# Performance work log

Measured on AMD Instinct MI355X. Metric: run time of the kernel, lower is better.

## Reference

```python
import jax, jax.numpy as jnp
import numpy as np
from jax import lax

B = 2; C = 256; NH = 8; NP = 4; NUM_LAYERS = 6; FFN = 1024
IN_SIZES = (512, 1024, 2048)
LVL_SHAPES = ((64, 64), (32, 32), (16, 16), (8, 8), (4, 4))
NL = len(LVL_SHAPES); DH = C // NH
N = sum(h * w for h, w in LVL_SHAPES)  # 5456 tokens over the pyramid


def _ln(x, g, b):
    m = x.mean(-1, keepdims=True)
    v = x.var(-1, keepdims=True)
    return (x - m) * lax.rsqrt(v + 1e-5) * g + b


def _gn(x, g, b, groups=8):
    Bb, Cc, Hh, Ww = x.shape
    xr = x.reshape(Bb, groups, Cc // groups, Hh, Ww)
    m = xr.mean((2, 3, 4), keepdims=True)
    v = xr.var((2, 3, 4), keepdims=True)
    xr = (xr - m) * lax.rsqrt(v + 1e-5)
    return xr.reshape(Bb, Cc, Hh, Ww) * g[None, :, None, None] + b[None, :, None, None]


def _conv(x, w, b, stride, pad):
    y = lax.conv_general_dilated(x, w, (stride, stride), [(pad, pad), (pad, pad)],
                                 dimension_numbers=('NCHW', 'OIHW', 'NCHW'))
    return y + b[None, :, None, None]


def _priors():
    # normalized (cx, cy) anchor centers per pyramid location
    pr = []
    for (fh, fw) in LVL_SHAPES:
        cy = (jnp.arange(fh, dtype=jnp.float32) + 0.5) / fh
        cx = (jnp.arange(fw, dtype=jnp.float32) + 0.5) / fw
        gy, gx = jnp.meshgrid(cy, cx, indexing='ij')
        pr.append(jnp.stack([gx, gy], -1).reshape(-1, 2))
    return jnp.concatenate(pr, 0)  # [N,2]


def _sample(vl, loc, fh, fw):
    # vl: [B,NH,S_l,DH] flattened level values; loc: [B,N,NH,NP,2] in [0,1]
    x = loc[..., 0] * fw - 0.5
    y = loc[..., 1] * fh - 0.5
    x0 = jnp.floor(x); y0 = jnp.floor(y)
    lx = x - x0; ly = y - y0

    def gather(xi, yi):
        inb = ((xi >= 0) & (xi <= fw - 1) & (yi >= 0) & (yi <= fh - 1)).astype(vl.dtype)
        xc = jnp.clip(xi, 0, fw - 1).astype(jnp.int32)
        yc = jnp.clip(yi, 0, fh - 1).astype(jnp.int32)
        idx = (yc * fw + xc).transpose(0, 2, 1, 3).reshape(B, NH, N * NP)
        g = jnp.take_along_axis(vl, idx[..., None], axis=2)  # [B,NH,N*NP,DH]
        g = g.reshape(B, NH, N, NP, DH).transpose(0, 2, 1, 3, 4)  # [B,N,NH,NP,DH]
        return g * inb[..., None]

    return (gather(x0, y0) * ((1 - lx) * (1 - ly))[..., None]
            + gather(x0 + 1, y0) * (lx * (1 - ly))[..., None]
            + gather(x0, y0 + 1) * ((1 - lx) * ly)[..., None]
            + gather(x0 + 1, y0 + 1) * (lx * ly)[..., None])


def _attn_layer(x, priors, g1, b1_, woff, boff, watt, batt, wval, bval, wout, bout):
    q = _ln(x, g1, b1_)
    off = (q @ woff + boff).reshape(B, N, NH, NL, NP, 2)
    att = jax.nn.softmax((q @ watt + batt).reshape(B, N, NH, NL * NP), axis=-1)
    att = att.reshape(B, N, NH, NL, NP)
    val = (q @ wval + bval).reshape(B, N, NH, DH)
    normz = jnp.array([[w, h] for (h, w) in LVL_SHAPES], jnp.float32)  # (W,H) per level
    loc = priors[None, :, None, None, None, :] + off / normz[None, None, None, :, None, :]
    out = jnp.zeros((B, N, NH, DH), x.dtype)
    start = 0
    for l, (fh, fw) in enumerate(LVL_SHAPES):
        vl = val[:, start:start + fh * fw].transpose(0, 2, 1, 3)  # [B,NH,S_l,DH]
        s = _sample(vl, loc[:, :, :, l], fh, fw)  # [B,N,NH,NP,DH]
        out = out + (s * att[:, :, :, l, :, None]).sum(3)
        start += fh * fw
    return x + out.reshape(B, N, C) @ wout + bout


def _ffn(x, g2, b2_, w1, b1_, w2, b2_2):
    h = jax.nn.relu(_ln(x, g2, b2_) @ w1 + b1_)
    return x + h @ w2 + b2_2


def _forward(in_map0, in_map1, in_map2, pw0, pb0, pw1, pb1, pw2, pb2,
             buw0, bub0, gng, gnb, buw1, bub1,
             ln1g, ln1b, woff, boff, watt, batt, wval, bval, wout, bout,
             ln2g, ln2b, w1, b1, w2, b2):
    maps = [_conv(in_map0, pw0, pb0, 1, 0), _conv(in_map1, pw1, pb1, 1, 0), _conv(in_map2, pw2, pb2, 1, 0)]
    m = _conv(in_map2, buw0, bub0, 2, 1)  # bottom-up from raw C5 (2048ch)
    maps.append(m)
    m = _conv(jax.nn.relu(_gn(m, gng, gnb)), buw1, bub1, 2, 1)
    maps.append(m)
    feats = jnp.concatenate([mm.reshape(B, C, -1).transpose(0, 2, 1) for mm in maps], axis=1)  # [B,N,C]
    priors = _priors()
    for i in range(NUM_LAYERS):
        feats = _attn_layer(feats, priors, ln1g[i], ln1b[i], woff[i], boff[i],
                            watt[i], batt[i], wval[i], bval[i], wout[i], bout[i])
        feats = _ffn(feats, ln2g[i], ln2b[i], w1[i], b1[i], w2[i], b2[i])
    return feats


def setup_inputs():
    key = jax.random.key(0)
    ks = list(jax.random.split(key, 40)); ki = iter(ks)
    def rn(shape, s=0.02):
        return jax.random.normal(next(ki), shape, jnp.float32) * s
    inp = {}
    for i, (cs, (h, w)) in enumerate(zip(IN_SIZES, LVL_SHAPES[:3])):
        inp[f"in_map{i}"] = jax.random.normal(next(ki), (B, cs, h, w), jnp.float32)
    for i, cs in enumerate(IN_SIZES):
        inp[f"pw{i}"] = rn((C, cs, 1, 1)); inp[f"pb{i}"] = jnp.zeros((C,), jnp.float32)
    inp["buw0"] = rn((C, IN_SIZES[-1], 3, 3)); inp["bub0"] = jnp.zeros((C,), jnp.float32)
    inp["gng"] = jnp.ones((C,), jnp.float32); inp["gnb"] = jnp.zeros((C,), jnp.float32)
    inp["buw1"] = rn((C, C, 3, 3)); inp["bub1"] = jnp.zeros((C,), jnp.float32)
    LYR = NUM_LAYERS
    inp["ln1g"] = jnp.ones((LYR, C), jnp.float32); inp["ln1b"] = jnp.zeros((LYR, C), jnp.float32)
    inp["woff"] = rn((LYR, C, NH * NL * NP * 2), 0.01)
    th = np.arange(NH) * (2.0 * np.pi / NH)
    grid = np.stack([np.cos(th), np.sin(th)], -1)
    grid = grid / np.abs(grid).max(-1, keepdims=True)  # [NH,2]
    boff = np.tile(grid[:, None, None, :], (1, NL, NP, 1)) * (np.arange(NP) + 1)[None, None, :, None]
    inp["boff"] = jnp.tile(jnp.asarray(boff.reshape(-1), jnp.float32)[None], (LYR, 1))
    inp["watt"] = rn((LYR, C, NH * NL * NP), 0.01); inp["batt"] = jnp.zeros((LYR, NH * NL * NP), jnp.float32)
    inp["wval"] = rn((LYR, C, C)); inp["bval"] = jnp.zeros((LYR, C), jnp.float32)
    inp["wout"] = rn((LYR, C, C)); inp["bout"] = jnp.zeros((LYR, C), jnp.float32)
    inp["ln2g"] = jnp.ones((LYR, C), jnp.float32); inp["ln2b"] = jnp.zeros((LYR, C), jnp.float32)
    inp["w1"] = rn((LYR, C, FFN)); inp["b1"] = jnp.zeros((LYR, FFN), jnp.float32)
    inp["w2"] = rn((LYR, FFN, C)); inp["b2"] = jnp.zeros((LYR, C), jnp.float32)
    return inp


def reference(in_map0, in_map1, in_map2, pw0, pb0, pw1, pb1, pw2, pb2,
              buw0, bub0, gng, gnb, buw1, bub1,
              ln1g, ln1b, woff, boff, watt, batt, wval, bval, wout, bout,
              ln2g, ln2b, w1, b1, w2, b2):
    feats = _forward(in_map0, in_map1, in_map2, pw0, pb0, pw1, pb1, pw2, pb2,
                     buw0, bub0, gng, gnb, buw1, bub1,
                     ln1g, ln1b, woff, boff, watt, batt, wval, bval, wout, bout,
                     ln2g, ln2b, w1, b1, w2, b2)
    outs = []
    start = 0
    for (fh, fw) in LVL_SHAPES:
        outs.append(feats[:, start:start + fh * fw].transpose(0, 2, 1).reshape(B, C, fh, fw))
        start += fh * fw
    return tuple(outs)
```

## Files before the change

### kernel.cpp

```cpp
#include <hip/hip_runtime.h>
#include <cstdint>

typedef long long i64;
typedef unsigned short u16;
typedef __attribute__((ext_vector_type(8))) short short8;
typedef __attribute__((ext_vector_type(8))) unsigned short us8;
typedef __attribute__((ext_vector_type(4))) float f32x4;

#define NTOK 5456
#define BNROWS 10912
#define NLAYERS 6

__device__ __forceinline__ u16 f2bf(float f) {
  unsigned u = __float_as_uint(f);
  return (u16)((u + 0x7FFFu + ((u >> 16) & 1u)) >> 16);
}
__device__ __forceinline__ float bf2f(u16 h) {
  return __uint_as_float(((unsigned)h) << 16);
}

template<int BNT>
__global__ __launch_bounds__(256) void mgemm_k(
    const u16* __restrict__ A, const u16* __restrict__ B, int K,
    float* __restrict__ C, float* __restrict__ C2, u16* __restrict__ C16, i64 sCm,
    const float* __restrict__ bias, int relu, int addres, int qkv,
    int M, int N, int mbsh, i64 bCz,
    int KS, float* __restrict__ part)
{
  constexpr int NW = BNT / 32;
  __shared__ u16 Asm[2][128 * 64];
  __shared__ u16 Bsm[2][BNT * 64];
  int tid = threadIdx.x;

  int bx = blockIdx.x, by = blockIdx.y;
  int gx = gridDim.x, gy = gridDim.y;
  int nwg = gx * gy;
  if (KS == 1 && nwg >= 16) {
    int lin = bx + gx * by;
    int xcd = lin & 7, k = lin >> 3;
    int q = nwg >> 3, r = nwg & 7;
    int f = (xcd < r) ? (xcd * (q + 1) + k) : (r * (q + 1) + (xcd - r) * q + k);
    bx = f / gy;
    by = f - bx * gy;
  }
  int m0 = bx * 128, n0 = by * BNT;

  int ks = blockIdx.z;
  int Kc = K / KS;
  int k0 = ks * Kc;
  int lane = tid & 63, w = tid >> 6;
  int wr = w >> 1, wc = w & 1;
  int r16 = lane & 15, g = lane >> 4;

  f32x4 acc[4][NW];
#pragma unroll
  for (int mi = 0; mi < 4; mi++)
#pragma unroll
    for (int nj = 0; nj < NW; nj++) acc[mi][nj] = (f32x4){0.f, 0.f, 0.f, 0.f};

  const u16* Ag = A + (i64)m0 * K + k0;
  const u16* Bg = B + (i64)n0 * K + k0;
  int nt = Kc >> 6;

  auto stage = [&](int buf, int kt) {
#pragma unroll
    for (int r = 0; r < 4; r++) {
      int s = r * 256 + tid;
      int row = s >> 3, c = s & 7;
      int cs = ((c ^ (row & 7)) << 3);
      __builtin_amdgcn_global_load_lds(
          (const __attribute__((address_space(1))) void*)(Ag + (i64)row * K + kt + cs),
          (__attribute__((address_space(3))) void*)(&Asm[buf][(r * 256 + (w << 6)) << 3]),
          16, 0, 0);
    }
#pragma unroll
    for (int r = 0; r < NW; r++) {
      int s = r * 256 + tid;
      int row = s >> 3, c = s & 7;
      int cs = ((c ^ (row & 7)) << 3);
      __builtin_amdgcn_global_load_lds(
          (const __attribute__((address_space(1))) void*)(Bg + (i64)row * K + kt + cs),
          (__attribute__((address_space(3))) void*)(&Bsm[buf][(r * 256 + (w << 6)) << 3]),
          16, 0, 0);
    }
  };

  stage(0, 0);
  __syncthreads();
  for (int t = 0; t < nt; t++) {
    int cur = t & 1;
    if (t + 1 < nt) stage(cur ^ 1, (t + 1) << 6);
#pragma unroll
    for (int h = 0; h < 2; h++) {
      short8 av[4], bv[NW];
#pragma unroll
      for (int mi = 0; mi < 4; mi++) {
        int row = wr * 64 + mi * 16 + r16;
        av[mi] = *(const short8*)&Asm[cur][row * 64 + ((((h << 2) + g) ^ (row & 7)) << 3)];
      }
#pragma unroll
      for (int nj = 0; nj < NW; nj++) {
        int row = wc * (NW * 16) + nj * 16 + r16;
        bv[nj] = *(const short8*)&Bsm[cur][row * 64 + ((((h << 2) + g) ^ (row & 7)) << 3)];
      }
#pragma unroll
      for (int mi = 0; mi < 4; mi++)
#pragma unroll
        for (int nj = 0; nj < NW; nj++)
          acc[mi][nj] = __builtin_amdgcn_mfma_f32_16x16x32_bf16(
              av[mi], bv[nj], acc[mi][nj], 0, 0, 0);
    }
    __syncthreads();
  }

  if (KS > 1) {
#pragma unroll
    for (int mi = 0; mi < 4; mi++)
#pragma unroll
      for (int nj = 0; nj < NW; nj++)
#pragma unroll
        for (int r = 0; r < 4; r++) {
          int grow = m0 + wr * 64 + mi * 16 + g * 4 + r;
          int gcol = n0 + wc * (NW * 16) + nj * 16 + r16;
          if (grow < M) part[((i64)ks * M + grow) * N + gcol] = acc[mi][nj][r];
        }
  } else if (qkv) {
    u16* off16 = (u16*)C;
    u16* att16 = (u16*)C2;
#pragma unroll
    for (int mi = 0; mi < 4; mi++)
#pragma unroll
      for (int nj = 0; nj < NW; nj++)
#pragma unroll
        for (int r = 0; r < 4; r++) {
          int grow = m0 + wr * 64 + mi * 16 + g * 4 + r;
          int gcol = n0 + wc * (NW * 16) + nj * 16 + r16;
          if (grow < M) {
            float v = acc[mi][nj][r] + bias[gcol];
            if (gcol < 320) off16[(i64)grow * 320 + gcol] = f2bf(v);
            else if (gcol < 480) att16[(i64)grow * 160 + (gcol - 320)] = f2bf(v);
            else if (gcol < 736) C16[(i64)grow * 256 + (gcol - 480)] = f2bf(v);
          }
        }
  } else {
    float bv[NW];
    int gc0 = n0 + wc * (NW * 16) + r16;
#pragma unroll
    for (int nj = 0; nj < NW; nj++)
      bv[nj] = bias ? bias[gc0 + nj * 16] : 0.f;
    int mask = (1 << mbsh) - 1;
#pragma unroll
    for (int mi = 0; mi < 4; mi++) {
#pragma unroll
      for (int r = 0; r < 4; r++) {
        int grow = m0 + wr * 64 + mi * 16 + g * 4 + r;
        if (grow >= M) continue;
        i64 rowb = (i64)(grow >> mbsh) * bCz + (i64)(grow & mask) * sCm;
#pragma unroll
        for (int nj = 0; nj < NW; nj++) {
          int gcol = gc0 + nj * 16;
          if (gcol >= N) continue;
          float v = acc[mi][nj][r] + bv[nj];
          if (relu) v = fmaxf(v, 0.f);
          i64 ci = rowb + gcol;
          if (C16) C16[ci] = f2bf(v);
          else {
            if (addres) v += C[ci];
            C[ci] = v;
          }
        }
      }
    }
  }
}

__global__ __launch_bounds__(512, 1) void ffn_fused_k(
    float* __restrict__ feats, const u16* __restrict__ w1n,
    const u16* __restrict__ w2n, const float* __restrict__ b1,
    const float* __restrict__ b2, const float* __restrict__ lng,
    const float* __restrict__ lnb, int M)
{
  __shared__ u16 B1s[2][64 * 256];
  __shared__ u16 B2s[2][256 * 64];
  __shared__ u16 Hs[64 * 88];
  __shared__ float b1s[1024];
  u16* As = &B1s[1][0];

  int tid = threadIdx.x;
  int lane = tid & 63, w = tid >> 6;
  int wr = w >> 1, wc = w & 1;
  int r16 = lane & 15, g = lane >> 4;
  int m0 = blockIdx.x * 64;

  auto stageW = [&](int buf, int ch) {
#pragma unroll
    for (int r = 0; r < 4; r++) {
      int s = r * 512 + tid;
      int row = s >> 5, c = s & 31;
      int cs = ((c ^ (row & 7)) << 3);
      __builtin_amdgcn_global_load_lds(
          (const __attribute__((address_space(1))) void*)(w1n + (i64)(ch * 64 + row) * 256 + cs),
          (__attribute__((address_space(3))) void*)(&B1s[buf][(r * 512 + (w << 6)) << 3]),
          16, 0, 0);
    }
#pragma unroll
    for (int r = 0; r < 4; r++) {
      int s = r * 512 + tid;
      int row = s >> 3, c = s & 7;
      int cs = ((c ^ (row & 7)) << 3);
      __builtin_amdgcn_global_load_lds(
          (const __attribute__((address_space(1))) void*)(w2n + (i64)row * 1024 + ch * 64 + cs),
          (__attribute__((address_space(3))) void*)(&B2s[buf][(r * 512 + (w << 6)) << 3]),
          16, 0, 0);
    }
  };

  stageW(0, 0);
  for (int i = tid; i < 1024; i += 512) b1s[i] = b1[i];

  {
    int rw = tid >> 3, c0 = (tid & 7) * 32;
    const float* fr = feats + (i64)(m0 + rw) * 256 + c0;
    float4 x[8];
    float s = 0.f, ss = 0.f;
#pragma unroll
    for (int j = 0; j < 8; j++) {
      x[j] = ((const float4*)fr)[j];
      s += x[j].x + x[j].y + x[j].z + x[j].w;
      ss += x[j].x * x[j].x + x[j].y * x[j].y + x[j].z * x[j].z + x[j].w * x[j].w;
    }
#pragma unroll
    for (int o = 1; o <= 4; o <<= 1) { s += __shfl_xor(s, o); ss += __shfl_xor(ss, o); }
    float mean = s * (1.f / 256.f);
    float rs = rsqrtf(ss * (1.f / 256.f) - mean * mean + 1e-5f);
    const float4* gp = (const float4*)(lng + c0);
    const float4* bp = (const float4*)(lnb + c0);
#pragma unroll
    for (int j = 0; j < 8; j += 2) {
      float4 g0 = gp[j], g1 = gp[j + 1];
      float4 b0 = bp[j], b1_ = bp[j + 1];
      us8 o;
      o[0] = f2bf((x[j].x - mean) * rs * g0.x + b0.x);
      o[1] = f2bf((x[j].y - mean) * rs * g0.y + b0.y);
      o[2] = f2bf((x[j].z - mean) * rs * g0.z + b0.z);
      o[3] = f2bf((x[j].w - mean) * rs * g0.w + b0.w);
      o[4] = f2bf((x[j + 1].x - mean) * rs * g1.x + b1_.x);
      o[5] = f2bf((x[j + 1].y - mean) * rs * g1.y + b1_.y);
      o[6] = f2bf((x[j + 1].z - mean) * rs * g1.z + b1_.z);
      o[7] = f2bf((x[j + 1].w - mean) * rs * g1.w + b1_.w);
      int gr = (tid & 7) * 4 + (j >> 1);
      *(us8*)&As[rw * 256 + ((gr ^ (rw & 7)) << 3)] = o;
    }
  }
  __syncthreads();

  short8 av_all[8];
  {
    int row = wr * 16 + r16;
#pragma unroll
    for (int ks = 0; ks < 8; ks++)
      av_all[ks] = *(const short8*)&As[row * 256 + (((ks * 4 + g) ^ (row & 7)) << 3)];
  }
  __syncthreads();

  f32x4 acc2[8];
#pragma unroll
  for (int nj = 0; nj < 8; nj++) acc2[nj] = (f32x4){0.f, 0.f, 0.f, 0.f};

  int cur = 0;
  for (int ch = 0; ch < 16; ch++) {
    if (ch + 1 < 16) stageW(cur ^ 1, ch + 1);

    f32x4 acc1[2];
#pragma unroll
    for (int nj = 0; nj < 2; nj++) acc1[nj] = (f32x4){0.f, 0.f, 0.f, 0.f};
#pragma unroll
    for (int ks = 0; ks < 8; ks++) {
      short8 bv[2];
#pragma unroll
      for (int nj = 0; nj < 2; nj++) {
        int row = wc * 32 + nj * 16 + r16;
        bv[nj] = *(const short8*)&B1s[cur][row * 256 + (((ks * 4 + g) ^ (row & 7)) << 3)];
      }
#pragma unroll
      for (int nj = 0; nj < 2; nj++)
        acc1[nj] = __builtin_amdgcn_mfma_f32_16x16x32_bf16(
            av_all[ks], bv[nj], acc1[nj], 0, 0, 0);
    }
#pragma unroll
    for (int nj = 0; nj < 2; nj++)
#pragma unroll
      for (int r = 0; r < 4; r++) {
        int hr = wr * 16 + g * 4 + r;
        int hc = wc * 32 + nj * 16 + r16;
        float v = acc1[nj][r] + b1s[ch * 64 + hc];
        Hs[hr * 88 + hc] = f2bf(fmaxf(v, 0.f));
      }
    __syncthreads();

#pragma unroll
    for (int hh = 0; hh < 2; hh++) {
      short8 av2 = *(const short8*)&Hs[(wr * 16 + r16) * 88 + hh * 32 + g * 8];
      short8 bv2[8];
#pragma unroll
      for (int nj = 0; nj < 8; nj++) {
        int n = wc * 128 + nj * 16 + r16;
        bv2[nj] = *(const short8*)&B2s[cur][n * 64 + (((hh * 4 + g) ^ (n & 7)) << 3)];
      }
#pragma unroll
      for (int nj = 0; nj < 8; nj++)
        acc2[nj] = __builtin_amdgcn_mfma_f32_16x16x32_bf16(
            av2, bv2[nj], acc2[nj], 0, 0, 0);
    }
    __syncthreads();
    cur ^= 1;
  }

#pragma unroll
  for (int r = 0; r < 4; r++) {
    int grow = m0 + wr * 16 + g * 4 + r;
    if (grow >= M) continue;
#pragma unroll
    for (int nj = 0; nj < 8; nj++) {
      int col = wc * 128 + nj * 16 + r16;
      i64 ci = (i64)grow * 256 + col;
      feats[ci] += acc2[nj][r] + b2[col];
    }
  }
}

__global__ void reduce_k(const float* __restrict__ part, float* __restrict__ C,
    const float* __restrict__ bias, int mbsh, i64 bCz, i64 sCm, int M, int N, int KS)
{
  int idx = blockIdx.x * 256 + threadIdx.x;
  if (idx >= M * N) return;
  int m = idx / N, n = idx - m * N;
  float v = bias ? bias[n] : 0.f;
  for (int ks = 0; ks < KS; ks++) v += part[((i64)ks * M + m) * N + n];
  C[(i64)(m >> mbsh) * bCz + (i64)(m & ((1 << mbsh) - 1)) * sCm + n] = v;
}

__global__ void cvt_w_pro_k(const float* __restrict__ pw0, const float* __restrict__ pw1,
    const float* __restrict__ pw2, const float* __restrict__ buw0,
    const float* __restrict__ buw1, u16* __restrict__ dst)
{
  int idx = blockIdx.x * 256 + threadIdx.x;
  if (idx >= 6225920) return;
  float v;
  if (idx < 131072) v = pw0[idx];
  else if (idx < 393216) v = pw1[idx - 131072];
  else if (idx < 917504) v = pw2[idx - 393216];
  else if (idx < 5636096) v = buw0[idx - 917504];
  else v = buw1[idx - 5636096];
  dst[idx] = f2bf(v);
}

__global__ void cvt_w_layer_k(const float* __restrict__ woff, const float* __restrict__ watt,
    const float* __restrict__ wval, const float* __restrict__ wout,
    const float* __restrict__ w1, const float* __restrict__ w2, u16* __restrict__ dst)
{
  int L = blockIdx.y;
  int o = blockIdx.x * 256 + threadIdx.x;
  if (o >= 786432) return;
  u16* d = dst + (i64)L * 786432;
  float v;
  if (o < 196608) {
    int n = o >> 8, k = o & 255;
    if (n < 320) v = woff[(i64)L * 81920 + k * 320 + n];
    else if (n < 480) v = watt[(i64)L * 40960 + k * 160 + (n - 320)];
    else if (n < 736) v = wval[(i64)L * 65536 + k * 256 + (n - 480)];
    else v = 0.f;
  } else if (o < 262144) {
    int o2 = o - 196608; int n = o2 >> 8, k = o2 & 255;
    v = wout[(i64)L * 65536 + k * 256 + n];
  } else if (o < 524288) {
    int o2 = o - 262144; int n = o2 >> 8, k = o2 & 255;
    v = w1[(i64)L * 262144 + (i64)k * 1024 + n];
  } else {
    int o2 = o - 524288; int n = o2 >> 10, k = o2 & 1023;
    v = w2[(i64)L * 262144 + (i64)k * 256 + n];
  }
  d[o] = f2bf(v);
}

__global__ void cvt_bias_k(const float* __restrict__ boff, const float* __restrict__ batt,
    const float* __restrict__ bval, float* __restrict__ bq)
{
  int idx = blockIdx.x * 256 + threadIdx.x;
  if (idx >= NLAYERS * 768) return;
  int L = idx / 768, n = idx - L * 768;
  float v;
  if (n < 320) v = boff[(i64)L * 320 + n];
  else if (n < 480) v = batt[(i64)L * 160 + (n - 320)];
  else if (n < 736) v = bval[(i64)L * 256 + (n - 480)];
  else v = 0.f;
  bq[idx] = v;
}

__global__ void cvt_a_proj_k(const float* __restrict__ in, u16* __restrict__ out,
                             int P, int K)
{
  i64 o = (i64)blockIdx.x * 256 + threadIdx.x;
  if (o >= (i64)2 * P * K) return;
  int m = (int)(o / K), k = (int)(o % K);
  int b = m / P, p = m - b * P;
  out[o] = f2bf(in[((i64)b * K + k) * P + p]);
}

__global__ void im2col_bf16_k(const float* __restrict__ in, u16* __restrict__ out,
    int Cin, int Hin, int Win, int Ho, int Wo)
{
  int Kk = Cin * 9;
  i64 total = (i64)2 * Ho * Wo * Kk;
  i64 o = (i64)blockIdx.x * 256 + threadIdx.x;
  if (o >= total) return;
  int k = (int)(o % Kk);
  int m = (int)(o / Kk);
  int hw = Ho * Wo;
  int b = m / hw, pix = m - b * hw;
  int oy = pix / Wo, ox = pix - oy * Wo;
  int ci = k / 9, r = k - ci * 9;
  int ky = r / 3, kx = r - ky * 3;
  int iy = oy * 2 - 1 + ky, ix = ox * 2 - 1 + kx;
  float v = 0.f;
  if (iy >= 0 && iy < Hin && ix >= 0 && ix < Win)
    v = in[(((i64)b * Cin + ci) * Hin + iy) * Win + ix];
  out[o] = f2bf(v);
}

__global__ void gn_relu_k(const float* __restrict__ feats, float* __restrict__ y,
    const float* __restrict__ g, const float* __restrict__ bt)
{
  int grp = blockIdx.x, b = blockIdx.y;
  int tid = threadIdx.x;
  const float* fb = feats + ((i64)b * NTOK + 5376) * 256 + grp * 32;
  float s = 0.f, ss = 0.f;
  for (int i = tid; i < 2048; i += 256) {
    int cl = i >> 6, p = i & 63;
    float v = fb[(i64)p * 256 + cl];
    s += v; ss += v * v;
  }
  __shared__ float sb[4], ssb[4];
#pragma unroll
  for (int o = 32; o > 0; o >>= 1) { s += __shfl_down(s, o); ss += __shfl_down(ss, o); }
  int wv = tid >> 6;
  if ((tid & 63) == 0) { sb[wv] = s; ssb[wv] = ss; }
  __syncthreads();
  float ts = sb[0] + sb[1] + sb[2] + sb[3];
  float tss = ssb[0] + ssb[1] + ssb[2] + ssb[3];
  float mean = ts * (1.f / 2048.f);
  float rs = rsqrtf(tss * (1.f / 2048.f) - mean * mean + 1e-5f);
  for (int i = tid; i < 2048; i += 256) {
    int cl = i >> 6, p = i & 63;
    int c = grp * 32 + cl;
    float v = (fb[(i64)p * 256 + cl] - mean) * rs * g[c] + bt[c];
    y[((i64)b * 256 + c) * 64 + p] = fmaxf(v, 0.f);
  }
}

__global__ __launch_bounds__(256) void ln_k(const float* __restrict__ x,
    u16* __restrict__ y, const float* __restrict__ g, const float* __restrict__ bt,
    int rows)
{
  int row = blockIdx.x * 4 + (threadIdx.x >> 6);
  if (row >= rows) return;
  int lane = threadIdx.x & 63;
  float4 v = ((const float4*)(x + (i64)row * 256))[lane];
  float s = v.x + v.y + v.z + v.w;
  float ss = v.x * v.x + v.y * v.y + v.z * v.z + v.w * v.w;
#pragma unroll
  for (int o = 32; o > 0; o >>= 1) { s += __shfl_down(s, o); ss += __shfl_down(ss, o); }
  s = __shfl(s, 0);
  ss = __shfl(ss, 0);
  float mean = s * (1.f / 256.f);
  float rs = rsqrtf(ss * (1.f / 256.f) - mean * mean + 1e-5f);
  float4 gg = ((const float4*)g)[lane];
  float4 bb = ((const float4*)bt)[lane];
  ushort4 o4;
  o4.x = f2bf((v.x - mean) * rs * gg.x + bb.x);
  o4.y = f2bf((v.y - mean) * rs * gg.y + bb.y);
  o4.z = f2bf((v.z - mean) * rs * gg.z + bb.z);
  o4.w = f2bf((v.w - mean) * rs * gg.w + bb.w);
  ((ushort4*)(y + (i64)row * 256))[lane] = o4;
}

__global__ __launch_bounds__(256) void dsample_k(
    const u16* __restrict__ val, const u16* __restrict__ off,
    const u16* __restrict__ att, u16* __restrict__ out)
{
  const int FH[5] = {64, 32, 16, 8, 4};
  const int ST[5] = {0, 4096, 5120, 5376, 5440};
  int bid = blockIdx.x;
  int chunk = (bid & 7) * 86 + (bid >> 3);
  if (chunk >= 682) return;
  int lane = threadIdx.x & 63;
  int half = lane >> 5;
  int l32 = lane & 31;
  int t = chunk * 8 + ((threadIdx.x >> 6) << 1) + half;
  int b = blockIdx.y;
  int h = l32 >> 2, d4 = l32 & 3;

  int lv;
  if (t < 4096)      lv = 0;
  else if (t < 5120) lv = 1;
  else if (t < 5376) lv = 2;
  else if (t < 5440) lv = 3;
  else               lv = 4;
  int loc = t - ST[lv];
  int sh = 6 - lv;
  int py = loc >> sh, px = loc - (py << sh);
  float inv = 1.f / (float)FH[lv];
  float prx = (px + 0.5f) * inv, pry = (py + 0.5f) * inv;
  i64 bt = (i64)b * NTOK + t;
  const u16* offp = off + bt * 320 + h * 40;
  const u16* attp = att + bt * 160 + h * 20;
  const u16* vbase = val + ((i64)b * NTOK) * 256 + h * 32 + d4 * 8;

  float own_a[5], own_fx[5], own_fy[5];
  int own_pk[5];
  float mx = -1e30f;
#pragma unroll
  for (int j = 0; j < 5; j++) {
    float lg = bf2f(attp[d4 + 4 * j]);
    own_a[j] = lg;
    mx = fmaxf(mx, lg);
  }
  mx = fmaxf(mx, __shfl_xor(mx, 1));
  mx = fmaxf(mx, __shfl_xor(mx, 2));
  float sum = 0.f;
#pragma unroll
  for (int j = 0; j < 5; j++) {
    float e = __expf(own_a[j] - mx);
    own_a[j] = e;
    sum += e;
  }
  sum += __shfl_xor(sum, 1);
  sum += __shfl_xor(sum, 2);
  float rinv = 1.f / sum;
#pragma unroll
  for (int j = 0; j < 5; j++) {
    int p = d4 + 4 * j;
    own_a[j] *= rinv;
    unsigned opk = *(const unsigned*)(offp + 2 * p);
    float ox = bf2f((u16)(opk & 0xFFFF));
    float oy = bf2f((u16)(opk >> 16));
    float sff = (float)(64 >> j);
    float xx = prx * sff + ox - 0.5f;
    float yy = pry * sff + oy - 0.5f;
    float xf = floorf(xx), yf = floorf(yy);
    own_fx[j] = xx - xf;
    own_fy[j] = yy - yf;
    own_pk[j] = (((int)yf) << 16) | (((int)xf) & 0xFFFF);
  }

  float acc[8] = {0.f, 0.f, 0.f, 0.f, 0.f, 0.f, 0.f, 0.f};
#pragma unroll
  for (int p = 0; p < 20; p++) {
    const int j = p >> 2;
    const int sf = FH[j], st = ST[j];
    int src = (half << 5) | (h << 2) | (p & 3);
    float wa = __shfl(own_a[j], src);
    float fx = __shfl(own_fx[j], src);
    float fy = __shfl(own_fy[j], src);
    int pk = __shfl(own_pk[j], src);
    int x0 = (pk << 16) >> 16;
    int y0 = pk >> 16;
    float gx0 = wa - wa * fx, gx1 = wa * fx;
    float w00 = gx0 - gx0 * fy, w01 = gx0 * fy;
    float w10 = gx1 - gx1 * fy, w11 = gx1 * fy;
    bool xin0 = (x0 >= 0) & (x0 < sf), xin1 = (x0 + 1 >= 0) & (x0 + 1 < sf);
    bool yin0 = (y0 >= 0) & (y0 < sf), yin1 = (y0 + 1 >= 0) & (y0 + 1 < sf);
    int ibase = st + y0 * sf + x0;
#define FMA8(W, IDX) { \
      us8 v = *(const us8*)(vbase + (i64)(IDX) * 256); \
      acc[0] = fmaf(W, bf2f(v[0]), acc[0]); acc[1] = fmaf(W, bf2f(v[1]), acc[1]); \
      acc[2] = fmaf(W, bf2f(v[2]), acc[2]); acc[3] = fmaf(W, bf2f(v[3]), acc[3]); \
      acc[4] = fmaf(W, bf2f(v[4]), acc[4]); acc[5] = fmaf(W, bf2f(v[5]), acc[5]); \
      acc[6] = fmaf(W, bf2f(v[6]), acc[6]); acc[7] = fmaf(W, bf2f(v[7]), acc[7]); }
    if (xin0 & yin0) FMA8(w00, ibase);
    if (xin1 & yin0) FMA8(w10, ibase + 1);
    if (xin0 & yin1) FMA8(w01, ibase + sf);
    if (xin1 & yin1) FMA8(w11, ibase + sf + 1);
#undef FMA8
  }
  us8 o;
#pragma unroll
  for (int i = 0; i < 8; i++) o[i] = f2bf(acc[i]);
  *(us8*)(out + ((bt * 8 + h) * 32 + d4 * 8)) = o;
}

__global__ __launch_bounds__(256) void untranspose_all_k(
    const float* __restrict__ feats, float* __restrict__ out)
{
  int u = blockIdx.x;
  int pt0, start, S; i64 ooff;
  if (u < 128)      { pt0 = u;       start = 0;    S = 4096; ooff = 0; }
  else if (u < 160) { pt0 = u - 128; start = 4096; S = 1024; ooff = 2097152; }
  else if (u < 168) { pt0 = u - 160; start = 5120; S = 256;  ooff = 2621440; }
  else if (u < 170) { pt0 = u - 168; start = 5376; S = 64;   ooff = 2752512; }
  else              { pt0 = 0;       start = 5440; S = 16;   ooff = 2785280; }
  __shared__ float tile[32][33];
  int pt = pt0 * 32, ct = blockIdx.y * 32, b = blockIdx.z;
  int tx = threadIdx.x & 31, ty = threadIdx.x >> 5;
  for (int i = ty; i < 32; i += 8) {
    int p = pt + i;
    tile[i][tx] = (p < S) ? feats[((i64)b * NTOK + start + p) * 256 + ct + tx] : 0.f;
  }
  __syncthreads();
  for (int i = ty; i < 32; i += 8) {
    int c = ct + i, p = pt + tx;
    if (p < S) out[ooff + ((i64)b * 256 + c) * S + p] = tile[tx][i];
  }
}

extern "C" void kernel_launch(void* const* d_in, const int* in_sizes, int n_in,
                              void* d_out, int out_size, void* d_ws, size_t ws_size,
                              hipStream_t stream)
{
  const float* in0  = (const float*)d_in[0];
  const float* in1  = (const float*)d_in[1];
  const float* in2  = (const float*)d_in[2];
  const float* pw0  = (const float*)d_in[3];
  const float* pb0  = (const float*)d_in[4];
  const float* pw1  = (const float*)d_in[5];
  const float* pb1  = (const float*)d_in[6];
  const float* pw2  = (const float*)d_in[7];
  const float* pb2  = (const float*)d_in[8];
  const float* buw0 = (const float*)d_in[9];
  const float* bub0 = (const float*)d_in[10];
  const float* gng  = (const float*)d_in[11];
  const float* gnb  = (const float*)d_in[12];
  const float* buw1 = (const float*)d_in[13];
  const float* bub1 = (const float*)d_in[14];
  const float* ln1g = (const float*)d_in[15];
  const float* ln1b = (const float*)d_in[16];
  const float* woff = (const float*)d_in[17];
  const float* boff = (const float*)d_in[18];
  const float* watt = (const float*)d_in[19];
  const float* batt = (const float*)d_in[20];
  const float* wval = (const float*)d_in[21];
  const float* bval = (const float*)d_in[22];
  const float* wout = (const float*)d_in[23];
  const float* bout = (const float*)d_in[24];
  const float* ln2g = (const float*)d_in[25];
  const float* ln2b = (const float*)d_in[26];
  const float* w1   = (const float*)d_in[27];
  const float* b1   = (const float*)d_in[28];
  const float* w2   = (const float*)d_in[29];
  const float* b2   = (const float*)d_in[30];
  float* out = (float*)d_out;

  const i64 TC = (i64)NTOK * 256;

  float* ws    = (float*)d_ws;
  float* feats = ws;
  u16*   qb    = (u16*)(feats + 2793472);
  u16*   valb  = qb + 2818048;
  u16*   sampb = valb + 2818048;
  float* U     = (float*)(sampb + 2818048);
  u16*   off16 = (u16*)U;
  u16*   att16 = off16 + 3491840;
  u16*   abuf  = (u16*)U;
  float* part  = U + 2097152;
  u16*   wb    = (u16*)(U + 5637120);
  float* bqkv  = (float*)(wb + 10944512);
  float* m4gn  = bqkv + 4608;

  auto mg128 = [&](dim3 grid, const u16* A, const u16* B, int K,
                   float* C, float* C2, u16* C16, i64 sCm, const float* bias,
                   int relu, int addres, int qkv, int M, int N, int mbsh, i64 bCz, int KS) {
    mgemm_k<128><<<grid, dim3(256), 0, stream>>>(A, B, K, C, C2, C16, sCm, bias,
        relu, addres, qkv, M, N, mbsh, bCz, KS, part);
  };
  auto mg64 = [&](dim3 grid, const u16* A, const u16* B, int K,
                  float* C, u16* C16, i64 sCm, const float* bias,
                  int relu, int addres, int M, int N, int mbsh, i64 bCz, int KS) {
    mgemm_k<64><<<grid, dim3(256), 0, stream>>>(A, B, K, C, nullptr, C16, sCm, bias,
        relu, addres, 0, M, N, mbsh, bCz, KS, part);
  };

  cvt_w_pro_k<<<dim3(24320), dim3(256), 0, stream>>>(pw0, pw1, pw2, buw0, buw1, wb);
  cvt_w_layer_k<<<dim3(3072, NLAYERS), dim3(256), 0, stream>>>(
      woff, watt, wval, wout, w1, w2, wb + 6225920);
  cvt_bias_k<<<dim3(18), dim3(256), 0, stream>>>(boff, batt, bval, bqkv);

  cvt_a_proj_k<<<dim3(16384), dim3(256), 0, stream>>>(in0, abuf, 4096, 512);
  mg64(dim3(64, 4, 1), abuf, wb, 512, feats, nullptr, 256, pb0, 0, 0,
       8192, 256, 12, TC, 1);
  cvt_a_proj_k<<<dim3(8192), dim3(256), 0, stream>>>(in1, abuf, 1024, 1024);
  mg64(dim3(16, 4, 2), abuf, wb + 131072, 1024, nullptr, nullptr, 256, nullptr, 0, 0,
       2048, 256, 10, 0, 2);
  reduce_k<<<dim3(2048), dim3(256), 0, stream>>>(part, feats + (i64)4096 * 256, pb1,
      10, TC, 256, 2048, 256, 2);
  cvt_a_proj_k<<<dim3(4096), dim3(256), 0, stream>>>(in2, abuf, 256, 2048);
  mg64(dim3(4, 4, 4), abuf, wb + 393216, 2048, nullptr, nullptr, 256, nullptr, 0, 0,
       512, 256, 8, 0, 4);
  reduce_k<<<dim3(512), dim3(256), 0, stream>>>(part, feats + (i64)5120 * 256, pb2,
      8, TC, 256, 512, 256, 4);

  im2col_bf16_k<<<dim3(9216), dim3(256), 0, stream>>>(in2, abuf, 2048, 16, 16, 8, 8);
  mg64(dim3(1, 4, 16), abuf, wb + 917504, 18432, nullptr, nullptr, 256, nullptr, 0, 0,
       128, 256, 6, 0, 16);
  reduce_k<<<dim3(128), dim3(256), 0, stream>>>(part, feats + (i64)5376 * 256, bub0,
      6, TC, 256, 128, 256, 16);

  gn_relu_k<<<dim3(8, 2), dim3(256), 0, stream>>>(feats, m4gn, gng, gnb);
  im2col_bf16_k<<<dim3(288), dim3(256), 0, stream>>>(m4gn, abuf, 256, 8, 8, 4, 4);
  mg64(dim3(1, 4, 4), abuf, wb + 5636096, 2304, nullptr, nullptr, 256, nullptr, 0, 0,
       32, 256, 4, 0, 4);
  reduce_k<<<dim3(32), dim3(256), 0, stream>>>(part, feats + (i64)5440 * 256, bub1,
      4, TC, 256, 32, 256, 4);

  for (int i = 0; i < NLAYERS; i++) {
    const u16* wbL = wb + 6225920 + (i64)i * 786432;
    ln_k<<<dim3(2728), dim3(256), 0, stream>>>(feats, qb,
        ln1g + (i64)i * 256, ln1b + (i64)i * 256, BNROWS);
    mg128(dim3(86, 6, 1), qb, wbL, 256, (float*)off16, (float*)att16, valb, 0,
          bqkv + (i64)i * 768, 0, 0, 1, BNROWS, 768, 14, 0, 1);
    dsample_k<<<dim3(688, 2), dim3(256), 0, stream>>>(valb, off16, att16, sampb);
    mg64(dim3(86, 4, 1), sampb, wbL + 196608, 256, feats, nullptr, 256,
         bout + (i64)i * 256, 0, 1, BNROWS, 256, 14, 0, 1);
    ffn_fused_k<<<dim3(171), dim3(512), 0, stream>>>(feats, wbL + 262144,
        wbL + 524288, b1 + (i64)i * 1024, b2 + (i64)i * 256,
        ln2g + (i64)i * 256, ln2b + (i64)i * 256, BNROWS);
  }

  untranspose_all_k<<<dim3(171, 8, 2), dim3(256), 0, stream>>>(feats, out);
  (void)in_sizes; (void)n_in; (void)out_size; (void)ws_size;
}
```

Baseline: 957.4 us.

## Compute full 64-wide hidden chunk per wave to drop mid-loop barrier in fused FFN

Each wave now computes all 64 hidden columns of its 16-row slice in the first FFN GEMM, using swapped MFMA operands so results come out transposed. The hidden tile is written to a private per-wave LDS region with packed 32-bit stores. This removes the block-wide __syncthreads between the two GEMMs. The cost is that the first GEMM's work is duplicated across the two wc waves, doubling its MFMAs and weight reads from LDS.

```diff
diff --git a/kernel.cpp b/kernel.cpp
--- a/kernel.cpp
+++ b/kernel.cpp
@@ -4,12 +4,14 @@
 typedef long long i64;
 typedef unsigned short u16;
 typedef __attribute__((ext_vector_type(8))) short short8;
+typedef __attribute__((ext_vector_type(4))) short short4v;
 typedef __attribute__((ext_vector_type(8))) unsigned short us8;
 typedef __attribute__((ext_vector_type(4))) float f32x4;
 
 #define NTOK 5456
 #define BNROWS 10912
 #define NLAYERS 6
+#define HSTR 68
 
 __device__ __forceinline__ u16 f2bf(float f) {
   unsigned u = __float_as_uint(f);
@@ -182,7 +184,7 @@
 {
   __shared__ u16 B1s[2][64 * 256];
   __shared__ u16 B2s[2][256 * 64];
-  __shared__ u16 Hs[64 * 88];
+  __shared__ u16 Hs[8 * 16 * HSTR];
   __shared__ float b1s[1024];
   u16* As = &B1s[1][0];
 
@@ -267,40 +269,49 @@
 #pragma unroll
   for (int nj = 0; nj < 8; nj++) acc2[nj] = (f32x4){0.f, 0.f, 0.f, 0.f};
 
+  u16* Hw = &Hs[w * 16 * HSTR];
   int cur = 0;
   for (int ch = 0; ch < 16; ch++) {
     if (ch + 1 < 16) stageW(cur ^ 1, ch + 1);
 
-    f32x4 acc1[2];
-#pragma unroll
-    for (int nj = 0; nj < 2; nj++) acc1[nj] = (f32x4){0.f, 0.f, 0.f, 0.f};
+    f32x4 acc1[4];
+#pragma unroll
+    for (int fb = 0; fb < 4; fb++) acc1[fb] = (f32x4){0.f, 0.f, 0.f, 0.f};
 #pragma unroll
     for (int ks = 0; ks < 8; ks++) {
-      short8 bv[2];
-#pragma unroll
-      for (int nj = 0; nj < 2; nj++) {
-        int row = wc * 32 + nj * 16 + r16;
-        bv[nj] = *(const short8*)&B1s[cur][row * 256 + (((ks * 4 + g) ^ (row & 7)) << 3)];
+      short8 wv[4];
+#pragma unroll
+      for (int fb = 0; fb < 4; fb++) {
+        int row = fb * 16 + r16;
+        wv[fb] = *(const short8*)&B1s[cur][row * 256 + (((ks * 4 + g) ^ (row & 7)) << 3)];
       }
 #pragma unroll
-      for (int nj = 0; nj < 2; nj++)
-        acc1[nj] = __builtin_amdgcn_mfma_f32_16x16x32_bf16(
-            av_all[ks], bv[nj], acc1[nj], 0, 0, 0);
-    }
-#pragma unroll
-    for (int nj = 0; nj < 2; nj++)
-#pragma unroll
-      for (int r = 0; r < 4; r++) {
-        int hr = wr * 16 + g * 4 + r;
-        int hc = wc * 32 + nj * 16 + r16;
-        float v = acc1[nj][r] + b1s[ch * 64 + hc];
-        Hs[hr * 88 + hc] = f2bf(fmaxf(v, 0.f));
-      }
-    __syncthreads();
+      for (int fb = 0; fb < 4; fb++)
+        acc1[fb] = __builtin_amdgcn_mfma_f32_16x16x32_bf16(
+            wv[fb], av_all[ks], acc1[fb], 0, 0, 0);
+    }
+#pragma unroll
+    for (int fb = 0; fb < 4; fb++) {
+      int fbase = fb * 16 + g * 4;
+      const float* bp = &b1s[ch * 64 + fbase];
+      float v0 = fmaxf(acc1[fb][0] + bp[0], 0.f);
+      float v1 = fmaxf(acc1[fb][1] + bp[1], 0.f);
+      float v2 = fmaxf(acc1[fb][2] + bp[2], 0.f);
+      float v3 = fmaxf(acc1[fb][3] + bp[3], 0.f);
+      unsigned p01 = (unsigned)f2bf(v0) | ((unsigned)f2bf(v1) << 16);
+      unsigned p23 = (unsigned)f2bf(v2) | ((unsigned)f2bf(v3) << 16);
+      *(unsigned*)&Hw[r16 * HSTR + fbase] = p01;
+      *(unsigned*)&Hw[r16 * HSTR + fbase + 2] = p23;
+    }
 
 #pragma unroll
     for (int hh = 0; hh < 2; hh++) {
-      short8 av2 = *(const short8*)&Hs[(wr * 16 + r16) * 88 + hh * 32 + g * 8];
+      const u16* hp = &Hw[r16 * HSTR + hh * 32 + g * 8];
+      short4v lo = *(const short4v*)hp;
+      short4v hi = *(const short4v*)(hp + 4);
+      short8 av2;
+      av2[0] = lo[0]; av2[1] = lo[1]; av2[2] = lo[2]; av2[3] = lo[3];
+      av2[4] = hi[0]; av2[5] = hi[1]; av2[6] = hi[2]; av2[7] = hi[3];
       short8 bv2[8];
 #pragma unroll
       for (int nj = 0; nj < 8; nj++) {
```

After: 997.7 us. 1.04x slower.
